# Kernel optimization log

Hardware: AMD Instinct MI355X
Metric: run time of the kernel (lower is better)

The kernel has to match this reference:

```python
import jax, jax.numpy as jnp
import numpy as np


def _patch_points(P):
    # replicates: meshgrid(y,x,z, indexing='ij'); points = cat([zz, yy, xx], -1).reshape(-1,3)
    lin = jnp.linspace(-1.0, 1.0, P)
    a, b, c = jnp.meshgrid(lin, lin, lin, indexing='ij')  # all identical linspaces
    pts = jnp.stack([c, b, a], axis=-1).reshape(-1, 3)     # (P^3, 3)
    return pts


def _proj_locations(points, angles):
    # Tomographic projection geometry (generate_projections_location):
    # rotate points about the detector-vertical axis and keep in-plane coords.
    # points: (N,3); angles: (A,) radians. Returns (A, N, 2) grid coords (x, y)
    # in grid_sample convention (last dim: x indexes width, y indexes height).
    p0 = points[:, 0]
    p1 = points[:, 1]
    p2 = points[:, 2]
    c = jnp.cos(angles)[:, None]   # (A,1)
    s = jnp.sin(angles)[:, None]
    gx = p0[None, :] * c + p2[None, :] * s          # (A, N)
    gy = jnp.broadcast_to(p1[None, :], gx.shape)    # (A, N)
    return jnp.stack([gx, gy], axis=-1)             # (A, N, 2)


def _bilinear_sample(img, grid):
    # img: (C,H,W); grid: (N,2) in [-1,1], align_corners=True, padding zeros.
    C, H, W = img.shape
    ix = (grid[:, 0] + 1.0) * 0.5 * (W - 1)
    iy = (grid[:, 1] + 1.0) * 0.5 * (H - 1)
    ix0 = jnp.floor(ix)
    iy0 = jnp.floor(iy)
    ix1 = ix0 + 1.0
    iy1 = iy0 + 1.0
    wx1 = ix - ix0
    wx0 = 1.0 - wx1
    wy1 = iy - iy0
    wy0 = 1.0 - wy1

    def corner(iyc, ixc, w):
        valid = (ixc >= 0) & (ixc <= W - 1) & (iyc >= 0) & (iyc <= H - 1)
        xi = jnp.clip(ixc, 0, W - 1).astype(jnp.int32)
        yi = jnp.clip(iyc, 0, H - 1).astype(jnp.int32)
        return img[:, yi, xi] * (w * valid)[None, :]   # (C,N)

    return (corner(iy0, ix0, wy0 * wx0) + corner(iy0, ix1, wy0 * wx1)
            + corner(iy1, ix0, wy1 * wx0) + corner(iy1, ix1, wy1 * wx1))


def setup_inputs() -> dict:
    key = jax.random.key(0)
    k1, k2 = jax.random.split(key)
    B, A, P = 128, 121, 33
    x = jax.random.normal(k1, (B, A, P, P), dtype=jnp.float32)
    angles = jax.random.uniform(k2, (1, A), dtype=jnp.float32,
                                minval=0.0, maxval=2.0 * np.pi)
    return {"x": x, "angles": angles}


def reference(x, angles):
    B, A, P, _ = x.shape
    pts = _patch_points(P)                       # (P^3, 3)
    grids = _proj_locations(pts, angles[0])      # (A, P^3, 2)
    xs = jnp.transpose(x, (1, 0, 2, 3))          # (A, B, P, P)

    def body(acc, inp):
        xi, gi = inp                             # (B,P,P), (P^3,2)
        return acc + _bilinear_sample(xi, gi), None

    acc0 = jnp.zeros((B, P * P * P), dtype=x.dtype)
    acc, _ = jax.lax.scan(body, acc0, (xs, grids))
    x_fbp = acc.reshape(B, P, P, P) / A
    return x_fbp
```

## Files before the change

### kernel.cpp

```cpp
#include <hip/hip_runtime.h>
#include <hip/hip_fp16.h>
#include <math.h>


#define PDIM 33
#define PP   1089
#define A_   121
#define ROWW 47
#define PADL 7
#define BLK  384
#define NV   3

#if defined(__has_builtin)
#if __has_builtin(__builtin_amdgcn_fractf)
#define FRACTF(x) __builtin_amdgcn_fractf(x)
#endif
#endif
#ifndef FRACTF
#define FRACTF(x) ((x) - floorf(x))
#endif

__global__ void cs_kernel(const float* __restrict__ angles,
                          float2* __restrict__ csw, int A)
{
    int j = threadIdx.x;
    if (j < A) {
        float s, c;
        sincosf(angles[j], &s, &c);
        csw[j] = make_float2(c, s);
    }
}

__global__ __launch_bounds__(BLK)
void fbp_adjoint_kernel(const float* __restrict__ x,
                        const float2* __restrict__ csw,
                        const float* __restrict__ angles,
                        float* __restrict__ out,
                        float invA)
{
    __shared__ __half2 dr[A_ * ROWW];
    __shared__ float2  cs_lds[A_];

    const int t   = threadIdx.x;
    const int blk = blockIdx.x;
    const int hb  = blk / PDIM;
    const int i1  = blk - hb * PDIM;
    const int b0  = 2 * hb;

    const bool use_ws = (csw != nullptr);
    if (!use_ws) {
        for (int j = t; j < A_; j += BLK) {
            float s, c;
            sincosf(angles[j], &s, &c);
            cs_lds[j] = make_float2(c, s);
        }
    }

    const float* r0 = x + (size_t)b0 * (A_ * PP) + (size_t)i1 * PDIM;
    const float* r1 = r0 + (size_t)(A_ * PP);
    for (int e = t; e < A_ * ROWW; e += BLK) {
        int j = e / ROWW;
        int p = e - j * ROWW;
        int k = p - PADL;
        float f0 = 0.0f, f1 = 0.0f;
        if (k >= 0 && k < PDIM) {
            size_t o = (size_t)j * PP + k;
            f0 = r0[o];
            f1 = r1[o];
        }
        dr[e] = __halves2half2(__float2half_rn(f0), __float2half_rn(f1));
    }
    __syncthreads();

    float u0[NV], u2[NV], a0[NV], a1[NV];
#pragma unroll
    for (int nn = 0; nn < NV; ++nn) {
        int n  = t + nn * BLK;
        int nc = (n < PP) ? n : (PP - 1);
        int q0 = nc / PDIM;
        int q2 = nc - q0 * PDIM;
        u0[nn] = (float)(q0 - 16);
        u2[nn] = (float)(q2 - 16);
        a0[nn] = 0.0f;
        a1[nn] = 0.0f;
    }

#pragma unroll 2
    for (int j = 0; j < A_; ++j) {
        float2 cj = use_ws ? csw[j] : cs_lds[j];
        const __half2* base = &dr[j * ROWW];
#pragma unroll
        for (int nn = 0; nn < NV; ++nn) {
            float ixp = fmaf(u2[nn], cj.x, fmaf(u0[nn], cj.y, 23.0f));
            int   kp  = (int)ixp;
            float w1  = FRACTF(ixp);
            float w0  = 1.0f - w1;
            __half2 d0 = base[kp];
            __half2 d1 = base[kp + 1];
            a0[nn] = fmaf(__half2float(__low2half(d0)),  w0, a0[nn]);
            a0[nn] = fmaf(__half2float(__low2half(d1)),  w1, a0[nn]);
            a1[nn] = fmaf(__half2float(__high2half(d0)), w0, a1[nn]);
            a1[nn] = fmaf(__half2float(__high2half(d1)), w1, a1[nn]);
        }
    }

    float* ob0 = out + (size_t)b0 * (PDIM * PP) + (size_t)i1 * PDIM;
    float* ob1 = ob0 + (size_t)(PDIM * PP);
#pragma unroll
    for (int nn = 0; nn < NV; ++nn) {
        int n = t + nn * BLK;
        if (n < PP) {
            int q0 = n / PDIM;
            int q2 = n - q0 * PDIM;
            size_t o = (size_t)q0 * PP + q2;
            ob0[o] = a0[nn] * invA;
            ob1[o] = a1[nn] * invA;
        }
    }
}

extern "C" void kernel_launch(void* const* d_in, const int* in_sizes, int n_in,
                              void* d_out, int out_size, void* d_ws, size_t ws_size,
                              hipStream_t stream)
{
    const float* x      = (const float*)d_in[0];
    const float* angles = (const float*)d_in[1];
    float* out          = (float*)d_out;

    const int A = in_sizes[1];
    const int B = in_sizes[0] / (A * PP);

    float2* csw = nullptr;
    if (ws_size >= sizeof(float2) * (size_t)A) {
        csw = (float2*)d_ws;
        cs_kernel<<<1, 128, 0, stream>>>(angles, csw, A);
    }

    dim3 grid((B / 2) * PDIM);
    dim3 block(BLK);
    fbp_adjoint_kernel<<<grid, block, 0, stream>>>(x, csw, angles, out,
                                                   1.0f / (float)A);
}
```

Measured before the change: 213.3 us.

## Use persistent grid-stride blocks and packed fp16 dot2 for interpolation

Switches the launch to a fixed 1280-block persistent grid, with each block looping over several (batch-pair, row) slices and reusing its precomputed per-thread coordinates. The inner bilinear accumulation now packs the two weights into a half2 and uses byte permutes plus the fdot2 builtin, replacing four fp32 FMAs and conversions with two dot products per voxel. This cuts ALU work in the hot loop and block launch overhead. In exchange it adds an extra barrier per slice, and converting the weights to fp16 (round-toward-zero) loses some precision. Slice counts that do not divide evenly across the grid can leave some blocks with more work than others.

```diff
diff --git a/kernel.cpp b/kernel.cpp
--- a/kernel.cpp
+++ b/kernel.cpp
@@ -10,6 +10,9 @@
 #define PADL 7
 #define BLK  384
 #define NV   3
+#define GRID 1280
+
+typedef _Float16 h2v __attribute__((ext_vector_type(2)));
 
 #if defined(__has_builtin)
 #if __has_builtin(__builtin_amdgcn_fractf)
@@ -31,22 +34,23 @@
     }
 }
 
+__device__ __forceinline__ float fdot2u(unsigned int a, unsigned int b, float c)
+{
+    return __builtin_amdgcn_fdot2(__builtin_bit_cast(h2v, a),
+                                  __builtin_bit_cast(h2v, b), c, false);
+}
+
 __global__ __launch_bounds__(BLK)
 void fbp_adjoint_kernel(const float* __restrict__ x,
                         const float2* __restrict__ csw,
                         const float* __restrict__ angles,
                         float* __restrict__ out,
-                        float invA)
+                        int nslice, float invA)
 {
-    __shared__ __half2 dr[A_ * ROWW];
-    __shared__ float2  cs_lds[A_];
+    __shared__ unsigned int dr[A_ * ROWW];
+    __shared__ float2       cs_lds[A_];
 
-    const int t   = threadIdx.x;
-    const int blk = blockIdx.x;
-    const int hb  = blk / PDIM;
-    const int i1  = blk - hb * PDIM;
-    const int b0  = 2 * hb;
-
+    const int t = threadIdx.x;
     const bool use_ws = (csw != nullptr);
     if (!use_ws) {
         for (int j = t; j < A_; j += BLK) {
@@ -56,23 +60,7 @@
         }
     }
 
-    const float* r0 = x + (size_t)b0 * (A_ * PP) + (size_t)i1 * PDIM;
-    const float* r1 = r0 + (size_t)(A_ * PP);
-    for (int e = t; e < A_ * ROWW; e += BLK) {
-        int j = e / ROWW;
-        int p = e - j * ROWW;
-        int k = p - PADL;
-        float f0 = 0.0f, f1 = 0.0f;
-        if (k >= 0 && k < PDIM) {
-            size_t o = (size_t)j * PP + k;
-            f0 = r0[o];
-            f1 = r1[o];
-        }
-        dr[e] = __halves2half2(__float2half_rn(f0), __float2half_rn(f1));
-    }
-    __syncthreads();
-
-    float u0[NV], u2[NV], a0[NV], a1[NV];
+    float u0[NV], u2[NV];
 #pragma unroll
     for (int nn = 0; nn < NV; ++nn) {
         int n  = t + nn * BLK;
@@ -81,40 +69,67 @@
         int q2 = nc - q0 * PDIM;
         u0[nn] = (float)(q0 - 16);
         u2[nn] = (float)(q2 - 16);
-        a0[nn] = 0.0f;
-        a1[nn] = 0.0f;
     }
 
+    for (int slice = blockIdx.x; slice < nslice; slice += GRID) {
+        if (slice != (int)blockIdx.x) __syncthreads();
+
+        const int hb = slice / PDIM;
+        const int i1 = slice - hb * PDIM;
+        const int b0 = 2 * hb;
+
+        const float* r0 = x + (size_t)b0 * (A_ * PP) + (size_t)i1 * PDIM;
+        const float* r1 = r0 + (size_t)(A_ * PP);
+        for (int e = t; e < A_ * ROWW; e += BLK) {
+            int j = e / ROWW;
+            int p = e - j * ROWW;
+            int k = p - PADL;
+            float f0 = 0.0f, f1 = 0.0f;
+            if (k >= 0 && k < PDIM) {
+                size_t o = (size_t)j * PP + k;
+                f0 = r0[o];
+                f1 = r1[o];
+            }
+            dr[e] = __builtin_bit_cast(unsigned int,
+                        __halves2half2(__float2half_rn(f0), __float2half_rn(f1)));
+        }
+        __syncthreads();
+
+        float a0[NV] = {0.0f, 0.0f, 0.0f};
+        float a1[NV] = {0.0f, 0.0f, 0.0f};
+
 #pragma unroll 2
-    for (int j = 0; j < A_; ++j) {
-        float2 cj = use_ws ? csw[j] : cs_lds[j];
-        const __half2* base = &dr[j * ROWW];
+        for (int j = 0; j < A_; ++j) {
+            float2 cj = use_ws ? csw[j] : cs_lds[j];
+            const unsigned int* base = &dr[j * ROWW];
+#pragma unroll
+            for (int nn = 0; nn < NV; ++nn) {
+                float ixp = fmaf(u2[nn], cj.x, fmaf(u0[nn], cj.y, 23.0f));
+                int   kp  = (int)ixp;
+                float w1  = FRACTF(ixp);
+                unsigned int wp = __builtin_bit_cast(unsigned int,
+                                    __builtin_amdgcn_cvt_pkrtz(1.0f - w1, w1));
+                unsigned int d0 = base[kp];
+                unsigned int d1 = base[kp + 1];
+                unsigned int p0 = __builtin_amdgcn_perm(d1, d0, 0x05040100u);
+                unsigned int p1 = __builtin_amdgcn_perm(d1, d0, 0x07060302u);
+                a0[nn] = fdot2u(p0, wp, a0[nn]);
+                a1[nn] = fdot2u(p1, wp, a1[nn]);
+            }
+        }
+
+        float* ob0 = out + (size_t)b0 * (PDIM * PP) + (size_t)i1 * PDIM;
+        float* ob1 = ob0 + (size_t)(PDIM * PP);
 #pragma unroll
         for (int nn = 0; nn < NV; ++nn) {
-            float ixp = fmaf(u2[nn], cj.x, fmaf(u0[nn], cj.y, 23.0f));
-            int   kp  = (int)ixp;
-            float w1  = FRACTF(ixp);
-            float w0  = 1.0f - w1;
-            __half2 d0 = base[kp];
-            __half2 d1 = base[kp + 1];
-            a0[nn] = fmaf(__half2float(__low2half(d0)),  w0, a0[nn]);
-            a0[nn] = fmaf(__half2float(__low2half(d1)),  w1, a0[nn]);
-            a1[nn] = fmaf(__half2float(__high2half(d0)), w0, a1[nn]);
-            a1[nn] = fmaf(__half2float(__high2half(d1)), w1, a1[nn]);
-        }
-    }
-
-    float* ob0 = out + (size_t)b0 * (PDIM * PP) + (size_t)i1 * PDIM;
-    float* ob1 = ob0 + (size_t)(PDIM * PP);
-#pragma unroll
-    for (int nn = 0; nn < NV; ++nn) {
-        int n = t + nn * BLK;
-        if (n < PP) {
-            int q0 = n / PDIM;
-            int q2 = n - q0 * PDIM;
-            size_t o = (size_t)q0 * PP + q2;
-            ob0[o] = a0[nn] * invA;
-            ob1[o] = a1[nn] * invA;
+            int n = t + nn * BLK;
+            if (n < PP) {
+                int q0 = n / PDIM;
+                int q2 = n - q0 * PDIM;
+                size_t o = (size_t)q0 * PP + q2;
+                ob0[o] = a0[nn] * invA;
+                ob1[o] = a1[nn] * invA;
+            }
         }
     }
 }
@@ -129,6 +144,7 @@
 
     const int A = in_sizes[1];
     const int B = in_sizes[0] / (A * PP);
+    const int nslice = (B / 2) * PDIM;
 
     float2* csw = nullptr;
     if (ws_size >= sizeof(float2) * (size_t)A) {
@@ -136,8 +152,8 @@
         cs_kernel<<<1, 128, 0, stream>>>(angles, csw, A);
     }
 
-    dim3 grid((B / 2) * PDIM);
+    dim3 grid(GRID < nslice ? GRID : nslice);
     dim3 block(BLK);
     fbp_adjoint_kernel<<<grid, block, 0, stream>>>(x, csw, angles, out,
-                                                   1.0f / (float)A);
+                                                   nslice, 1.0f / (float)A);
 }
```

Measured after the change: 215.3 us. About the same (+0.9%).
